# Kernel optimization log

Measured on AMD Instinct MI355X. Metric: run time of the kernel, lower is better.

The kernel has to match this reference:

```python
import jax, jax.numpy as jnp
import numpy as np
from jax import lax

B, L = 2, 2048          # batch, seq_len
V = 256                 # vocab
DM = 256                # d_model
DI = 512                # d_inner = 2*d_model (expand=2)
N = 16                  # d_state
R = 16                  # dt_rank = ceil(d_model/16)
K = 4                   # d_conv
NL = 4                  # n_layer
DO = 10                 # d_output
EPS = 1e-5


def setup_inputs() -> dict:
    key = jax.random.key(0)
    ks = jax.random.split(key, 12)
    f = lambda k, shp, s=0.02: (jax.random.normal(k, shp, jnp.float32) * s)
    A_init = jnp.log(jnp.tile(jnp.arange(1, N + 1, dtype=jnp.float32)[None, None, :], (NL, DI, 1)))
    return {
        "input_ids": jax.random.randint(ks[0], (B, L), 0, V, dtype=jnp.int32),
        "emb": f(ks[1], (V, DM)),
        "norm_w": jnp.ones((NL, DM), jnp.float32),
        "norm_b": jnp.zeros((NL, DM), jnp.float32),
        "in_proj_w": f(ks[2], (NL, 2 * DI, DM)),
        "conv_w": f(ks[3], (NL, DI, K), 0.1),
        "conv_b": jnp.zeros((NL, DI), jnp.float32),
        "x_proj_w": f(ks[4], (NL, R + 2 * N, DI)),
        "dt_proj_w": f(ks[5], (NL, DI, R), 0.1),
        "dt_proj_b": f(ks[6], (NL, DI), 0.1),
        "A_log": A_init,
        "Dp": jnp.ones((NL, DI), jnp.float32),
        "out_proj_w": f(ks[7], (NL, DM, DI)),
        "normf_w": jnp.ones((DM,), jnp.float32),
        "normf_b": jnp.zeros((DM,), jnp.float32),
        "dec_w": f(ks[8], (DO, DM)),
        "dec_b": jnp.zeros((DO,), jnp.float32),
    }


def _layer_norm(x, w, b):
    m = x.mean(-1, keepdims=True)
    v = jnp.mean((x - m) ** 2, axis=-1, keepdims=True)
    return (x - m) * lax.rsqrt(v + EPS) * w + b


def _causal_dwconv(x, w, b):
    # x: [B,L,DI], w: [DI,K] depthwise causal conv
    xt = x.transpose(0, 2, 1)  # [B,DI,L]
    out = lax.conv_general_dilated(xt, w[:, None, :], (1,), [(K - 1, 0)],
                                   feature_group_count=DI)
    return (out + b[None, :, None]).transpose(0, 2, 1)


def _selective_scan(deltaA, deltaBu, C):
    # deltaA, deltaBu: [B,L,DI,N]; C: [B,L,N]
    def step(h, inp):
        dA, dBu, c = inp
        h = dA * h + dBu                       # [B,DI,N]
        y = jnp.einsum('bdn,bn->bd', h, c)
        return h, y
    h0 = jnp.zeros(deltaA.shape[:1] + deltaA.shape[2:], deltaA.dtype)
    _, ys = lax.scan(step, h0, (deltaA.transpose(1, 0, 2, 3),
                                deltaBu.transpose(1, 0, 2, 3),
                                C.transpose(1, 0, 2)))
    return ys.transpose(1, 0, 2)  # [B,L,DI]


def _mixer(x, in_w, cw, cb, xp_w, dt_w, dt_b, A_log, Dp, out_w):
    xz = jnp.einsum('bld,ed->ble', x, in_w)        # [B,L,2*DI]
    xm, z = jnp.split(xz, 2, axis=-1)
    xc = jax.nn.silu(_causal_dwconv(xm, cw, cb))   # [B,L,DI]
    x_dbl = jnp.einsum('bld,ed->ble', xc, xp_w)    # [B,L,R+2N]
    dt, Bm, Cm = jnp.split(x_dbl, [R, R + N], axis=-1)
    delta = jax.nn.softplus(jnp.einsum('blr,dr->bld', dt, dt_w) + dt_b)  # [B,L,DI]
    A = -jnp.exp(A_log)                            # [DI,N]
    deltaA = jnp.exp(delta[..., None] * A)         # [B,L,DI,N]
    deltaBu = delta[..., None] * Bm[:, :, None, :] * xc[..., None]
    y = _selective_scan(deltaA, deltaBu, Cm)       # [B,L,DI]
    y = y + Dp * xc
    y = y * jax.nn.silu(z)
    return jnp.einsum('bld,ed->ble', y, out_w)     # [B,L,DM]


def reference(input_ids, emb, norm_w, norm_b, in_proj_w, conv_w, conv_b,
              x_proj_w, dt_proj_w, dt_proj_b, A_log, Dp, out_proj_w,
              normf_w, normf_b, dec_w, dec_b):
    hidden = emb[input_ids]                        # [B,L,DM]
    residual = None
    for i in range(NL):
        residual = hidden + residual if residual is not None else hidden
        h = _layer_norm(residual, norm_w[i], norm_b[i])
        hidden = _mixer(h, in_proj_w[i], conv_w[i], conv_b[i], x_proj_w[i],
                        dt_proj_w[i], dt_proj_b[i], A_log[i], Dp[i], out_proj_w[i])
    residual = hidden + residual
    hidden = _layer_norm(residual, normf_w, normf_b)
    pooled = hidden.mean(axis=1)                   # [B,DM]
    return pooled @ dec_w.T + dec_b                # [B,DO]
```

## Files before the change

kernel.cpp:

```cpp
#include <hip/hip_runtime.h>
#include <hip/hip_bf16.h>

#define BB 2
#define LL 2048
#define DM 256
#define DI 512
#define NST 16
#define RDT 16
#define KC 4
#define NLAY 4
#define DOUT 10
#define XDIM 48
#define TOK (BB*LL)
#define EPSF 1e-5f
#define CHUNK 16
#define NCH (LL/CHUNK)

typedef __bf16 bf16x8 __attribute__((ext_vector_type(8)));
typedef __bf16 bf16x4 __attribute__((ext_vector_type(4)));
typedef float  f32x4  __attribute__((ext_vector_type(4)));

__device__ __forceinline__ float sigmoid_f(float x) { return 1.0f / (1.0f + __expf(-x)); }

__global__ void cast_w_kernel(const float* __restrict__ a, const float* __restrict__ b,
                              const float* __restrict__ c,
                              __bf16* __restrict__ ab, __bf16* __restrict__ bb,
                              __bf16* __restrict__ cbf,
                              int na, int nb, int nc) {
  int stride = gridDim.x * 256;
  for (int i = blockIdx.x*256 + threadIdx.x; i < na; i += stride) ab[i] = (__bf16)a[i];
  for (int i = blockIdx.x*256 + threadIdx.x; i < nb; i += stride) bb[i] = (__bf16)b[i];
  for (int i = blockIdx.x*256 + threadIdx.x; i < nc; i += stride) cbf[i] = (__bf16)c[i];
}

__global__ void add_ln_kernel(float* __restrict__ residual, const float* __restrict__ hidden,
                              const int* __restrict__ ids, const float* __restrict__ emb,
                              const float* __restrict__ w, const float* __restrict__ bia,
                              float* __restrict__ out, __bf16* __restrict__ out_bf,
                              int first, int write32) {
  int t = blockIdx.x, d = threadIdx.x;
  __shared__ float ws8[8];
  float r;
  if (first) r = emb[ids[t]*DM + d];
  else       r = hidden[t*DM + d] + residual[t*DM + d];
  residual[t*DM + d] = r;
  float s = r;
  #pragma unroll
  for (int o = 32; o; o >>= 1) s += __shfl_down(s, o);
  if ((d & 63) == 0) ws8[d >> 6] = s;
  __syncthreads();
  float mean = (ws8[0] + ws8[1] + ws8[2] + ws8[3]) * (1.0f/DM);
  float diff = r - mean;
  float q = diff * diff;
  #pragma unroll
  for (int o = 32; o; o >>= 1) q += __shfl_down(q, o);
  if ((d & 63) == 0) ws8[4 + (d >> 6)] = q;
  __syncthreads();
  float var = (ws8[4] + ws8[5] + ws8[6] + ws8[7]) * (1.0f/DM);
  float v = diff * rsqrtf(var + EPSF) * w[d] + bia[d];
  if (write32) out[t*DM + d] = v;
  out_bf[t*DM + d] = (__bf16)v;
}

__global__ __launch_bounds__(256, 2) void gemm_in_bf16(const __bf16* __restrict__ A,
                                                       const __bf16* __restrict__ W,
                                                       __bf16* __restrict__ xm,
                                                       __bf16* __restrict__ zg) {
  __shared__ __bf16 As[4*64*8];
  __shared__ __bf16 Ws[8*64*8];
  const int K = DM;
  int tid = threadIdx.x;
  int lane = tid & 63, wv = tid >> 6;
  int bm = blockIdx.y * 64, be = blockIdx.x * 128;
  int ss = tid >> 6, sq = (tid >> 4) & 3, sm = tid & 15;
  f32x4 acc[8];
  #pragma unroll
  for (int et = 0; et < 8; ++et) acc[et] = (f32x4){0.f, 0.f, 0.f, 0.f};
  for (int k0 = 0; k0 < K; k0 += 32) {
    bf16x8 av = *(const bf16x8*)&A[(size_t)(bm + ss*16 + sm)*K + k0 + sq*8];
    bf16x8 w0 = *(const bf16x8*)&W[(size_t)(be + ss*16 + sm)*K + k0 + sq*8];
    bf16x8 w1 = *(const bf16x8*)&W[(size_t)(be + 64 + ss*16 + sm)*K + k0 + sq*8];
    __syncthreads();
    *(bf16x8*)&As[((ss*4 + sq)*16 + sm)*8] = av;
    *(bf16x8*)&Ws[((ss*4 + sq)*16 + sm)*8] = w0;
    *(bf16x8*)&Ws[(((4 + ss)*4 + sq)*16 + sm)*8] = w1;
    __syncthreads();
    bf16x8 af = *(const bf16x8*)&As[(wv*64 + lane)*8];
    #pragma unroll
    for (int et = 0; et < 8; ++et) {
      bf16x8 bfr = *(const bf16x8*)&Ws[(et*64 + lane)*8];
      acc[et] = __builtin_amdgcn_mfma_f32_16x16x32_bf16(af, bfr, acc[et], 0, 0, 0);
    }
  }
  int row0 = bm + wv*16 + (lane >> 4)*4;
  int colb = lane & 15;
  #pragma unroll
  for (int et = 0; et < 8; ++et) {
    int col = be + et*16 + colb;
    if (col < DI) {
      #pragma unroll
      for (int r = 0; r < 4; ++r)
        xm[(size_t)(row0 + r)*DI + col] = (__bf16)acc[et][r];
    } else {
      #pragma unroll
      for (int r = 0; r < 4; ++r) {
        float zv = acc[et][r];
        zg[(size_t)(row0 + r)*DI + col - DI] = (__bf16)(zv * sigmoid_f(zv));
      }
    }
  }
}

__global__ __launch_bounds__(256, 2) void gemm_out_bf16(const __bf16* __restrict__ A,
                                                        const __bf16* __restrict__ W,
                                                        float* __restrict__ C) {
  __shared__ __bf16 As[4*64*8];
  __shared__ __bf16 Ws[4*64*8];
  const int K = DI, E = DM;
  int tid = threadIdx.x;
  int lane = tid & 63, wv = tid >> 6;
  int bm = blockIdx.y * 64, be = blockIdx.x * 64;
  int ss = tid >> 6, sq = (tid >> 4) & 3, sm = tid & 15;
  f32x4 acc[4];
  #pragma unroll
  for (int et = 0; et < 4; ++et) acc[et] = (f32x4){0.f, 0.f, 0.f, 0.f};
  for (int k0 = 0; k0 < K; k0 += 32) {
    bf16x8 av = *(const bf16x8*)&A[(size_t)(bm + ss*16 + sm)*K + k0 + sq*8];
    bf16x8 wvv = *(const bf16x8*)&W[(size_t)(be + ss*16 + sm)*K + k0 + sq*8];
    __syncthreads();
    *(bf16x8*)&As[((ss*4 + sq)*16 + sm)*8] = av;
    *(bf16x8*)&Ws[((ss*4 + sq)*16 + sm)*8] = wvv;
    __syncthreads();
    bf16x8 af = *(const bf16x8*)&As[(wv*64 + lane)*8];
    #pragma unroll
    for (int et = 0; et < 4; ++et) {
      bf16x8 bfr = *(const bf16x8*)&Ws[(et*64 + lane)*8];
      acc[et] = __builtin_amdgcn_mfma_f32_16x16x32_bf16(af, bfr, acc[et], 0, 0, 0);
    }
  }
  int row0 = bm + wv*16 + (lane >> 4)*4;
  int col0 = be + (lane & 15);
  #pragma unroll
  for (int et = 0; et < 4; ++et)
    #pragma unroll
    for (int r = 0; r < 4; ++r)
      C[(size_t)(row0 + r)*E + col0 + et*16] = acc[et][r];
}

__global__ __launch_bounds__(512, 2) void xproj16(const __bf16* __restrict__ xm,
                                                  const float* __restrict__ cw,
                                                  const float* __restrict__ cb,
                                                  const __bf16* __restrict__ Wbf,
                                                  float* __restrict__ out,
                                                  __bf16* __restrict__ xc) {
  __shared__ float red[8][3][16][16];
  int tid = threadIdx.x;
  int lane = tid & 63, w = tid >> 6;
  int bm = blockIdx.x * 16;
  int row = bm + (lane & 15);
  int l = row & (LL - 1);
  int kg = (lane >> 4) * 8;
  f32x4 acc[3];
  #pragma unroll
  for (int e = 0; e < 3; ++e) acc[e] = (f32x4){0.f, 0.f, 0.f, 0.f};
  #pragma unroll
  for (int ks = 0; ks < 2; ++ks) {
    int ch = w*64 + ks*32 + kg;
    bf16x8 v0 = *(const bf16x8*)&xm[(size_t)row*DI + ch];
    bf16x8 v1 = (l >= 1) ? *(const bf16x8*)&xm[(size_t)(row-1)*DI + ch] : (bf16x8)(__bf16)0;
    bf16x8 v2 = (l >= 2) ? *(const bf16x8*)&xm[(size_t)(row-2)*DI + ch] : (bf16x8)(__bf16)0;
    bf16x8 v3 = (l >= 3) ? *(const bf16x8*)&xm[(size_t)(row-3)*DI + ch] : (bf16x8)(__bf16)0;
    bf16x8 a8;
    #pragma unroll
    for (int j = 0; j < 8; ++j) {
      float4 cwv = *(const float4*)&cw[(ch + j)*KC];
      float cv = cb[ch + j];
      cv = fmaf(cwv.x, (float)v3[j], cv);
      cv = fmaf(cwv.y, (float)v2[j], cv);
      cv = fmaf(cwv.z, (float)v1[j], cv);
      cv = fmaf(cwv.w, (float)v0[j], cv);
      a8[j] = (__bf16)(cv * sigmoid_f(cv));
    }
    *(bf16x8*)&xc[(size_t)row*DI + ch] = a8;
    #pragma unroll
    for (int e = 0; e < 3; ++e) {
      bf16x8 bv = *(const bf16x8*)&Wbf[(size_t)(e*16 + (lane & 15))*DI + ch];
      acc[e] = __builtin_amdgcn_mfma_f32_16x16x32_bf16(a8, bv, acc[e], 0, 0, 0);
    }
  }
  #pragma unroll
  for (int e = 0; e < 3; ++e)
    #pragma unroll
    for (int r = 0; r < 4; ++r)
      red[w][e][(lane >> 4)*4 + r][lane & 15] = acc[e][r];
  __syncthreads();
  for (int idx = tid; idx < 768; idx += 512) {
    int e = idx >> 8, rr = (idx >> 4) & 15, cc = idx & 15;
    float s = 0.f;
    #pragma unroll
    for (int w8 = 0; w8 < 8; ++w8) s += red[w8][e][rr][cc];
    out[(size_t)(bm + rr)*XDIM + e*16 + cc] = s;
  }
}

__global__ __launch_bounds__(256) void scan_pass1(
    const __bf16* __restrict__ xc, const float* __restrict__ xdbl,
    const float* __restrict__ dtw, const float* __restrict__ dtb,
    const float* __restrict__ A_log, const float* __restrict__ Dp,
    float* __restrict__ hloc, float* __restrict__ dsum,
    float* __restrict__ ylocal, float* __restrict__ csout) {
  __shared__ __align__(16) float DBC[CHUNK][48];
  int bc = blockIdx.x >> 1;
  int d  = ((blockIdx.x & 1) << 8) + threadIdx.x;
  int b = bc >> 7, c = bc & (NCH-1);
  int t0 = b*LL + c*CHUNK;
  int tid = threadIdx.x;
  if (tid < CHUNK*12) {
    int row = tid / 12, q = tid - row*12;
    *(float4*)&DBC[row][q*4] = *(const float4*)&xdbl[(size_t)(t0+row)*XDIM + q*4];
  }
  __syncthreads();
  float4 wq[4];
  #pragma unroll
  for (int i = 0; i < 4; ++i) wq[i] = *(const float4*)&dtw[(size_t)d*RDT + i*4];
  float dtbv = dtb[d];
  float Dpv = Dp[d];
  float A[NST];
  #pragma unroll
  for (int n = 0; n < NST; ++n) A[n] = -__expf(A_log[d*NST + n]);
  float A0 = A[0];
  bool geo = true;
  #pragma unroll
  for (int n = 1; n < NST; ++n) {
    float ideal = A0 * (float)(n+1);
    geo = geo && (fabsf(A[n] - ideal) <= 1e-5f * fabsf(ideal));
  }
  float h[NST];
  #pragma unroll
  for (int n = 0; n < NST; ++n) h[n] = 0.f;
  float ds = 0.f;
  for (int l = 0; l < CHUNK; ++l) {
    int t = t0 + l;
    float xcv = (float)xc[(size_t)t*DI + d];
    float acc = dtbv;
    #pragma unroll
    for (int i = 0; i < 4; ++i) {
      float4 a = *(const float4*)&DBC[l][i*4];
      acc = fmaf(a.x, wq[i].x, acc); acc = fmaf(a.y, wq[i].y, acc);
      acc = fmaf(a.z, wq[i].z, acc); acc = fmaf(a.w, wq[i].w, acc);
    }
    float del = fmaxf(acc, 0.f) + log1pf(__expf(-fabsf(acc)));
    ds += del;
    float dx = del * xcv;
    float yv = 0.f;
    if (geo) {
      float e = __expf(del * A0);
      float dA = e;
      h[0] = fmaf(dA, h[0], dx * DBC[l][16]);
      yv = fmaf(h[0], DBC[l][32], yv);
      #pragma unroll
      for (int n = 1; n < NST; ++n) {
        dA *= e;
        h[n] = fmaf(dA, h[n], dx * DBC[l][16 + n]);
        yv = fmaf(h[n], DBC[l][32 + n], yv);
      }
    } else {
      #pragma unroll
      for (int n = 0; n < NST; ++n) {
        h[n] = fmaf(__expf(del * A[n]), h[n], dx * DBC[l][16 + n]);
        yv = fmaf(h[n], DBC[l][32 + n], yv);
      }
    }
    yv = fmaf(Dpv, xcv, yv);
    ylocal[(size_t)t*DI + d] = yv;
    csout[(size_t)t*DI + d] = ds;
  }
  #pragma unroll
  for (int n = 0; n < NST; ++n)
    hloc[((size_t)(b*NST + n)*NCH + c)*DI + d] = h[n];
  dsum[(size_t)bc*DI + d] = ds;
}

__global__ __launch_bounds__(256) void scan_pass2(
    const float* __restrict__ hloc, const float* __restrict__ dsum,
    const float* __restrict__ A_log, float* __restrict__ hinit) {
  int g = blockIdx.x*256 + threadIdx.x;
  int d = g & (DI-1);
  int n = (g >> 9) & (NST-1);
  int b = g >> 13;
  float A = -__expf(A_log[d*NST + n]);
  float hc = 0.f;
  size_t base = (size_t)(b*NST + n)*NCH*DI + d;
  #pragma unroll 4
  for (int c = 0; c < NCH; ++c) {
    hinit[base + (size_t)c*DI] = hc;
    float P = __expf(A * dsum[(size_t)(b*NCH + c)*DI + d]);
    hc = fmaf(P, hc, hloc[base + (size_t)c*DI]);
  }
}

__global__ __launch_bounds__(256) void scan_pass3(
    const float* __restrict__ cs, const float* __restrict__ ylocal,
    const __bf16* __restrict__ zg, const float* __restrict__ xdbl,
    const float* __restrict__ A_log, const float* __restrict__ hinit,
    __bf16* __restrict__ y) {
  __shared__ __align__(16) float Cs[CHUNK][16];
  int bc = blockIdx.x >> 1;
  int d  = ((blockIdx.x & 1) << 8) + threadIdx.x;
  int b = bc >> 7, c = bc & (NCH-1);
  int t0 = b*LL + c*CHUNK;
  int tid = threadIdx.x;
  if (tid < CHUNK*4) {
    int row = tid >> 2, q = tid & 3;
    *(float4*)&Cs[row][q*4] = *(const float4*)&xdbl[(size_t)(t0+row)*XDIM + 32 + q*4];
  }
  __syncthreads();
  float A[NST];
  #pragma unroll
  for (int n = 0; n < NST; ++n) A[n] = -__expf(A_log[d*NST + n]);
  float A0 = A[0];
  bool geo = true;
  #pragma unroll
  for (int n = 1; n < NST; ++n) {
    float ideal = A0 * (float)(n+1);
    geo = geo && (fabsf(A[n] - ideal) <= 1e-5f * fabsf(ideal));
  }
  float hin[NST];
  #pragma unroll
  for (int n = 0; n < NST; ++n) hin[n] = hinit[((size_t)(b*NST + n)*NCH + c)*DI + d];
  for (int l = 0; l < CHUNK; ++l) {
    int t = t0 + l;
    float csv = cs[(size_t)t*DI + d];
    float ylv = ylocal[(size_t)t*DI + d];
    float zvg = (float)zg[(size_t)t*DI + d];
    float corr = 0.f;
    if (geo) {
      float g = __expf(csv * A0);
      float dA = g;
      corr = hin[0] * dA * Cs[l][0];
      #pragma unroll
      for (int n = 1; n < NST; ++n) {
        dA *= g;
        corr = fmaf(hin[n] * dA, Cs[l][n], corr);
      }
    } else {
      #pragma unroll
      for (int n = 0; n < NST; ++n)
        corr = fmaf(hin[n] * __expf(A[n] * csv), Cs[l][n], corr);
    }
    y[(size_t)t*DI + d] = (__bf16)((ylv + corr) * zvg);
  }
}

__global__ void pool1_kernel(const float* __restrict__ ln, float* __restrict__ part) {
  int blk = blockIdx.x;
  int b = blk >> 7, c = blk & 127;
  int d = threadIdx.x;
  const float* base = ln + (size_t)b*LL*DM + (size_t)c*16*DM + d;
  float s = 0.f;
  #pragma unroll
  for (int l = 0; l < 16; ++l) s += base[(size_t)l*DM];
  part[(size_t)blk*DM + d] = s;
}

__global__ void pool_decode_kernel(const float* __restrict__ part, const float* __restrict__ dw,
                                   const float* __restrict__ db, float* __restrict__ out) {
  int b = blockIdx.x, d = threadIdx.x;
  __shared__ float pooled[DM];
  float s = 0.f;
  for (int c = 0; c < 128; ++c) s += part[(size_t)(b*128 + c)*DM + d];
  pooled[d] = s * (1.0f/LL);
  __syncthreads();
  if (d < DOUT) {
    float acc = db[d];
    for (int m = 0; m < DM; ++m) acc = fmaf(pooled[m], dw[d*DM + m], acc);
    out[b*DOUT + d] = acc;
  }
}

extern "C" void kernel_launch(void* const* d_in, const int* in_sizes, int n_in,
                              void* d_out, int out_size, void* d_ws, size_t ws_size,
                              hipStream_t stream) {
  const int*   ids     = (const int*)d_in[0];
  const float* emb     = (const float*)d_in[1];
  const float* norm_w  = (const float*)d_in[2];
  const float* norm_b  = (const float*)d_in[3];
  const float* in_w    = (const float*)d_in[4];
  const float* conv_w  = (const float*)d_in[5];
  const float* conv_b  = (const float*)d_in[6];
  const float* xp_w    = (const float*)d_in[7];
  const float* dt_w    = (const float*)d_in[8];
  const float* dt_b    = (const float*)d_in[9];
  const float* A_log   = (const float*)d_in[10];
  const float* Dp      = (const float*)d_in[11];
  const float* out_w   = (const float*)d_in[12];
  const float* normf_w = (const float*)d_in[13];
  const float* normf_b = (const float*)d_in[14];
  const float* dec_w   = (const float*)d_in[15];
  const float* dec_b   = (const float*)d_in[16];
  float* out = (float*)d_out;

  float* ws = (float*)d_ws;
  float* hidden   = ws; ws += TOK*DM;
  float* residual = ws; ws += TOK*DM;
  float* hbuf     = ws; ws += TOK*DM;
  float* xdblbuf  = ws; ws += TOK*XDIM;
  float* hlocbuf  = ws; ws += (size_t)BB*NCH*NST*DI;
  float* hinitbuf = ws; ws += (size_t)BB*NCH*NST*DI;
  float* dsumbuf  = ws; ws += (size_t)BB*NCH*DI;
  float* partbuf  = ws; ws += (size_t)BB*128*DM;
  float* csbuf    = ws; ws += (size_t)TOK*DI;
  float* ylbuf    = ws; ws += (size_t)TOK*DI;
  __bf16* xmbuf   = (__bf16*)ws; ws += TOK*DI/2;
  __bf16* zgbuf   = (__bf16*)ws; ws += TOK*DI/2;
  __bf16* xcbuf   = (__bf16*)ws; ws += TOK*DI/2;
  __bf16* hbuf_bf = (__bf16*)ws; ws += TOK*DM/2;
  __bf16* ybuf_bf = (__bf16*)ws; ws += TOK*DI/2;
  __bf16* inw_bf  = (__bf16*)ws; ws += (size_t)NLAY*2*DI*DM/2;
  __bf16* outw_bf = (__bf16*)ws; ws += (size_t)NLAY*DM*DI/2;
  __bf16* xpw_bf  = (__bf16*)ws; ws += (size_t)NLAY*XDIM*DI/2 + 256;

  const int n_inw = NLAY*2*DI*DM, n_outw = NLAY*DM*DI, n_xpw = NLAY*XDIM*DI;
  cast_w_kernel<<<2048, 256, 0, stream>>>(in_w, out_w, xp_w, inw_bf, outw_bf, xpw_bf,
                                          n_inw, n_outw, n_xpw);

  for (int i = 0; i < NLAY; ++i) {
    add_ln_kernel<<<TOK, DM, 0, stream>>>(residual, hidden, ids, emb,
                                          norm_w + i*DM, norm_b + i*DM,
                                          hbuf, hbuf_bf, i == 0, 0);
    gemm_in_bf16<<<dim3((2*DI)/128, TOK/64), 256, 0, stream>>>(
        hbuf_bf, inw_bf + (size_t)i*2*DI*DM, xmbuf, zgbuf);
    xproj16<<<TOK/16, 512, 0, stream>>>(
        xmbuf, conv_w + i*DI*KC, conv_b + i*DI,
        xpw_bf + (size_t)i*XDIM*DI, xdblbuf, xcbuf);
    scan_pass1<<<BB*NCH*(DI/256), 256, 0, stream>>>(
        xcbuf, xdblbuf,
        dt_w + (size_t)i*DI*RDT, dt_b + i*DI, A_log + (size_t)i*DI*NST,
        Dp + i*DI, hlocbuf, dsumbuf, ylbuf, csbuf);
    scan_pass2<<<(BB*NST*DI)/256, 256, 0, stream>>>(
        hlocbuf, dsumbuf, A_log + (size_t)i*DI*NST, hinitbuf);
    scan_pass3<<<BB*NCH*(DI/256), 256, 0, stream>>>(
        csbuf, ylbuf, zgbuf, xdblbuf, A_log + (size_t)i*DI*NST,
        hinitbuf, ybuf_bf);
    gemm_out_bf16<<<dim3(DM/64, TOK/64), 256, 0, stream>>>(
        ybuf_bf, outw_bf + (size_t)i*DM*DI, hidden);
  }

  add_ln_kernel<<<TOK, DM, 0, stream>>>(residual, hidden, ids, emb,
                                        normf_w, normf_b, hbuf, hbuf_bf, 0, 1);
  pool1_kernel<<<BB*128, DM, 0, stream>>>(hbuf, partbuf);
  pool_decode_kernel<<<BB, DM, 0, stream>>>(partbuf, dec_w, dec_b, out);
}
```

Before: 432.5 us.

## Replace LDS-tiled GEMMs with direct-load MFMA kernels and shrink scan_pass2 blocks

The in-projection and out-projection GEMMs drop shared-memory staging and barriers. Each wave now loads its A and W fragments straight from global memory into MFMA operands, using 16-row tiles and more blocks. scan_pass2 uses 64-thread blocks so its 16384 threads spread over more CUs. The aim is to remove sync and LDS overhead and raise parallelism, at the cost of redundant global and L2 reads of the weight fragments across blocks.

```diff
diff --git a/kernel.cpp b/kernel.cpp
--- a/kernel.cpp
+++ b/kernel.cpp
@@ -62,89 +62,74 @@
   out_bf[t*DM + d] = (__bf16)v;
 }
 
-__global__ __launch_bounds__(256, 2) void gemm_in_bf16(const __bf16* __restrict__ A,
-                                                       const __bf16* __restrict__ W,
-                                                       __bf16* __restrict__ xm,
-                                                       __bf16* __restrict__ zg) {
-  __shared__ __bf16 As[4*64*8];
-  __shared__ __bf16 Ws[8*64*8];
-  const int K = DM;
+__global__ __launch_bounds__(512, 4) void gemm_in_d(const __bf16* __restrict__ A,
+                                                    const __bf16* __restrict__ W,
+                                                    __bf16* __restrict__ xm,
+                                                    __bf16* __restrict__ zg) {
   int tid = threadIdx.x;
   int lane = tid & 63, wv = tid >> 6;
-  int bm = blockIdx.y * 64, be = blockIdx.x * 128;
-  int ss = tid >> 6, sq = (tid >> 4) & 3, sm = tid & 15;
-  f32x4 acc[8];
-  #pragma unroll
-  for (int et = 0; et < 8; ++et) acc[et] = (f32x4){0.f, 0.f, 0.f, 0.f};
-  for (int k0 = 0; k0 < K; k0 += 32) {
-    bf16x8 av = *(const bf16x8*)&A[(size_t)(bm + ss*16 + sm)*K + k0 + sq*8];
-    bf16x8 w0 = *(const bf16x8*)&W[(size_t)(be + ss*16 + sm)*K + k0 + sq*8];
-    bf16x8 w1 = *(const bf16x8*)&W[(size_t)(be + 64 + ss*16 + sm)*K + k0 + sq*8];
-    __syncthreads();
-    *(bf16x8*)&As[((ss*4 + sq)*16 + sm)*8] = av;
-    *(bf16x8*)&Ws[((ss*4 + sq)*16 + sm)*8] = w0;
-    *(bf16x8*)&Ws[(((4 + ss)*4 + sq)*16 + sm)*8] = w1;
-    __syncthreads();
-    bf16x8 af = *(const bf16x8*)&As[(wv*64 + lane)*8];
-    #pragma unroll
-    for (int et = 0; et < 8; ++et) {
-      bf16x8 bfr = *(const bf16x8*)&Ws[(et*64 + lane)*8];
-      acc[et] = __builtin_amdgcn_mfma_f32_16x16x32_bf16(af, bfr, acc[et], 0, 0, 0);
-    }
-  }
-  int row0 = bm + wv*16 + (lane >> 4)*4;
-  int colb = lane & 15;
-  #pragma unroll
-  for (int et = 0; et < 8; ++et) {
-    int col = be + et*16 + colb;
-    if (col < DI) {
+  int bm = blockIdx.y * 16;
+  int row = bm + (lane & 15);
+  int kg = (lane >> 4) * 8;
+  int be = blockIdx.x * 512 + wv * 64;
+  f32x4 acc[4];
+  #pragma unroll
+  for (int e = 0; e < 4; ++e) acc[e] = (f32x4){0.f, 0.f, 0.f, 0.f};
+  for (int k0 = 0; k0 < DM; k0 += 32) {
+    bf16x8 av = *(const bf16x8*)&A[(size_t)row*DM + k0 + kg];
+    #pragma unroll
+    for (int e = 0; e < 4; ++e) {
+      bf16x8 bv = *(const bf16x8*)&W[(size_t)(be + e*16 + (lane & 15))*DM + k0 + kg];
+      acc[e] = __builtin_amdgcn_mfma_f32_16x16x32_bf16(av, bv, acc[e], 0, 0, 0);
+    }
+  }
+  int r0 = bm + (lane >> 4)*4;
+  int cb = lane & 15;
+  if (blockIdx.x == 0) {
+    #pragma unroll
+    for (int e = 0; e < 4; ++e)
       #pragma unroll
       for (int r = 0; r < 4; ++r)
-        xm[(size_t)(row0 + r)*DI + col] = (__bf16)acc[et][r];
-    } else {
+        xm[(size_t)(r0 + r)*DI + be + e*16 + cb] = (__bf16)acc[e][r];
+  } else {
+    int ze = be - DI;
+    #pragma unroll
+    for (int e = 0; e < 4; ++e)
       #pragma unroll
       for (int r = 0; r < 4; ++r) {
-        float zv = acc[et][r];
-        zg[(size_t)(row0 + r)*DI + col - DI] = (__bf16)(zv * sigmoid_f(zv));
+        float zv = acc[e][r];
+        zg[(size_t)(r0 + r)*DI + ze + e*16 + cb] = (__bf16)(zv * sigmoid_f(zv));
       }
-    }
-  }
-}
-
-__global__ __launch_bounds__(256, 2) void gemm_out_bf16(const __bf16* __restrict__ A,
-                                                        const __bf16* __restrict__ W,
-                                                        float* __restrict__ C) {
-  __shared__ __bf16 As[4*64*8];
-  __shared__ __bf16 Ws[4*64*8];
-  const int K = DI, E = DM;
+  }
+}
+
+__global__ __launch_bounds__(256, 4) void gemm_out_d(const __bf16* __restrict__ A,
+                                                     const __bf16* __restrict__ W,
+                                                     float* __restrict__ C) {
   int tid = threadIdx.x;
   int lane = tid & 63, wv = tid >> 6;
-  int bm = blockIdx.y * 64, be = blockIdx.x * 64;
-  int ss = tid >> 6, sq = (tid >> 4) & 3, sm = tid & 15;
-  f32x4 acc[4];
-  #pragma unroll
-  for (int et = 0; et < 4; ++et) acc[et] = (f32x4){0.f, 0.f, 0.f, 0.f};
-  for (int k0 = 0; k0 < K; k0 += 32) {
-    bf16x8 av = *(const bf16x8*)&A[(size_t)(bm + ss*16 + sm)*K + k0 + sq*8];
-    bf16x8 wvv = *(const bf16x8*)&W[(size_t)(be + ss*16 + sm)*K + k0 + sq*8];
-    __syncthreads();
-    *(bf16x8*)&As[((ss*4 + sq)*16 + sm)*8] = av;
-    *(bf16x8*)&Ws[((ss*4 + sq)*16 + sm)*8] = wvv;
-    __syncthreads();
-    bf16x8 af = *(const bf16x8*)&As[(wv*64 + lane)*8];
-    #pragma unroll
-    for (int et = 0; et < 4; ++et) {
-      bf16x8 bfr = *(const bf16x8*)&Ws[(et*64 + lane)*8];
-      acc[et] = __builtin_amdgcn_mfma_f32_16x16x32_bf16(af, bfr, acc[et], 0, 0, 0);
-    }
-  }
-  int row0 = bm + wv*16 + (lane >> 4)*4;
-  int col0 = be + (lane & 15);
-  #pragma unroll
-  for (int et = 0; et < 4; ++et)
+  int bm = blockIdx.y * 16;
+  int row = bm + (lane & 15);
+  int kg = (lane >> 4) * 8;
+  int be = blockIdx.x * 128 + wv * 32;
+  f32x4 acc[2];
+  #pragma unroll
+  for (int e = 0; e < 2; ++e) acc[e] = (f32x4){0.f, 0.f, 0.f, 0.f};
+  for (int k0 = 0; k0 < DI; k0 += 32) {
+    bf16x8 av = *(const bf16x8*)&A[(size_t)row*DI + k0 + kg];
+    #pragma unroll
+    for (int e = 0; e < 2; ++e) {
+      bf16x8 bv = *(const bf16x8*)&W[(size_t)(be + e*16 + (lane & 15))*DI + k0 + kg];
+      acc[e] = __builtin_amdgcn_mfma_f32_16x16x32_bf16(av, bv, acc[e], 0, 0, 0);
+    }
+  }
+  int r0 = bm + (lane >> 4)*4;
+  int cb = lane & 15;
+  #pragma unroll
+  for (int e = 0; e < 2; ++e)
     #pragma unroll
     for (int r = 0; r < 4; ++r)
-      C[(size_t)(row0 + r)*E + col0 + et*16] = acc[et][r];
+      C[(size_t)(r0 + r)*DM + be + e*16 + cb] = acc[e][r];
 }
 
 __global__ __launch_bounds__(512, 2) void xproj16(const __bf16* __restrict__ xm,
@@ -281,10 +266,10 @@
   dsum[(size_t)bc*DI + d] = ds;
 }
 
-__global__ __launch_bounds__(256) void scan_pass2(
+__global__ __launch_bounds__(64) void scan_pass2(
     const float* __restrict__ hloc, const float* __restrict__ dsum,
     const float* __restrict__ A_log, float* __restrict__ hinit) {
-  int g = blockIdx.x*256 + threadIdx.x;
+  int g = blockIdx.x*64 + threadIdx.x;
   int d = g & (DI-1);
   int n = (g >> 9) & (NST-1);
   int b = g >> 13;
@@ -428,7 +413,7 @@
     add_ln_kernel<<<TOK, DM, 0, stream>>>(residual, hidden, ids, emb,
                                           norm_w + i*DM, norm_b + i*DM,
                                           hbuf, hbuf_bf, i == 0, 0);
-    gemm_in_bf16<<<dim3((2*DI)/128, TOK/64), 256, 0, stream>>>(
+    gemm_in_d<<<dim3(2, TOK/16), 512, 0, stream>>>(
         hbuf_bf, inw_bf + (size_t)i*2*DI*DM, xmbuf, zgbuf);
     xproj16<<<TOK/16, 512, 0, stream>>>(
         xmbuf, conv_w + i*DI*KC, conv_b + i*DI,
@@ -437,12 +422,12 @@
         xcbuf, xdblbuf,
         dt_w + (size_t)i*DI*RDT, dt_b + i*DI, A_log + (size_t)i*DI*NST,
         Dp + i*DI, hlocbuf, dsumbuf, ylbuf, csbuf);
-    scan_pass2<<<(BB*NST*DI)/256, 256, 0, stream>>>(
+    scan_pass2<<<(BB*NST*DI)/64, 64, 0, stream>>>(
         hlocbuf, dsumbuf, A_log + (size_t)i*DI*NST, hinitbuf);
     scan_pass3<<<BB*NCH*(DI/256), 256, 0, stream>>>(
         csbuf, ylbuf, zgbuf, xdblbuf, A_log + (size_t)i*DI*NST,
         hinitbuf, ybuf_bf);
-    gemm_out_bf16<<<dim3(DM/64, TOK/64), 256, 0, stream>>>(
+    gemm_out_d<<<dim3(2, TOK/16), 256, 0, stream>>>(
         ybuf_bf, outw_bf + (size_t)i*DM*DI, hidden);
   }
 
```

Measured after the change: 482.0 us. 11.5% more time.

## Fuse conv/x-projection with first scan pass, keep xc in shared memory

Applied to the files above, without the earlier changes.

Merges the conv+SiLU+x_proj kernel with the chunk-local scan pass so each 512-thread block handles one 16-token chunk. The conv output xc stays in XOR-swizzled shared memory and the x_proj results go straight into the shared DBC tile, so xc no longer makes a round trip through global memory and one kernel launch per layer goes away. Separately, scan_pass2 now uses 64-thread blocks to spread its 16K threads over more workgroups. The cost is a fused kernel with more shared memory, no occupancy hint in its launch bounds, and 512 threads per block doing the sequential scan, which may lower occupancy.

```diff
diff --git a/kernel.cpp b/kernel.cpp
--- a/kernel.cpp
+++ b/kernel.cpp
@@ -147,19 +147,27 @@
       C[(size_t)(row0 + r)*E + col0 + et*16] = acc[et][r];
 }
 
-__global__ __launch_bounds__(512, 2) void xproj16(const __bf16* __restrict__ xm,
-                                                  const float* __restrict__ cw,
-                                                  const float* __restrict__ cb,
-                                                  const __bf16* __restrict__ Wbf,
-                                                  float* __restrict__ out,
-                                                  __bf16* __restrict__ xc) {
+__global__ __launch_bounds__(512) void xproj_scan1(
+    const __bf16* __restrict__ xm, const float* __restrict__ cw,
+    const float* __restrict__ cb, const __bf16* __restrict__ Wbf,
+    const float* __restrict__ dtw, const float* __restrict__ dtb,
+    const float* __restrict__ A_log, const float* __restrict__ Dp,
+    float* __restrict__ xdbl, float* __restrict__ hloc,
+    float* __restrict__ dsum, float* __restrict__ ylocal,
+    float* __restrict__ csout) {
   __shared__ float red[8][3][16][16];
+  __shared__ __bf16 xc_s[CHUNK][DI];
+  __shared__ __align__(16) float DBC[CHUNK][48];
   int tid = threadIdx.x;
   int lane = tid & 63, w = tid >> 6;
-  int bm = blockIdx.x * 16;
-  int row = bm + (lane & 15);
+  int bc = blockIdx.x;
+  int t0 = bc * CHUNK;
+  int b = bc >> 7, c = bc & (NCH - 1);
+  int r16 = lane & 15;
+  int row = t0 + r16;
   int l = row & (LL - 1);
   int kg = (lane >> 4) * 8;
+
   f32x4 acc[3];
   #pragma unroll
   for (int e = 0; e < 3; ++e) acc[e] = (f32x4){0.f, 0.f, 0.f, 0.f};
@@ -181,10 +189,10 @@
       cv = fmaf(cwv.w, (float)v0[j], cv);
       a8[j] = (__bf16)(cv * sigmoid_f(cv));
     }
-    *(bf16x8*)&xc[(size_t)row*DI + ch] = a8;
+    *(bf16x8*)&xc_s[r16][ch ^ ((r16 & 7) << 3)] = a8;
     #pragma unroll
     for (int e = 0; e < 3; ++e) {
-      bf16x8 bv = *(const bf16x8*)&Wbf[(size_t)(e*16 + (lane & 15))*DI + ch];
+      bf16x8 bv = *(const bf16x8*)&Wbf[(size_t)(e*16 + r16)*DI + ch];
       acc[e] = __builtin_amdgcn_mfma_f32_16x16x32_bf16(a8, bv, acc[e], 0, 0, 0);
     }
   }
@@ -192,34 +200,19 @@
   for (int e = 0; e < 3; ++e)
     #pragma unroll
     for (int r = 0; r < 4; ++r)
-      red[w][e][(lane >> 4)*4 + r][lane & 15] = acc[e][r];
+      red[w][e][(lane >> 4)*4 + r][r16] = acc[e][r];
   __syncthreads();
   for (int idx = tid; idx < 768; idx += 512) {
     int e = idx >> 8, rr = (idx >> 4) & 15, cc = idx & 15;
     float s = 0.f;
     #pragma unroll
     for (int w8 = 0; w8 < 8; ++w8) s += red[w8][e][rr][cc];
-    out[(size_t)(bm + rr)*XDIM + e*16 + cc] = s;
-  }
-}
-
-__global__ __launch_bounds__(256) void scan_pass1(
-    const __bf16* __restrict__ xc, const float* __restrict__ xdbl,
-    const float* __restrict__ dtw, const float* __restrict__ dtb,
-    const float* __restrict__ A_log, const float* __restrict__ Dp,
-    float* __restrict__ hloc, float* __restrict__ dsum,
-    float* __restrict__ ylocal, float* __restrict__ csout) {
-  __shared__ __align__(16) float DBC[CHUNK][48];
-  int bc = blockIdx.x >> 1;
-  int d  = ((blockIdx.x & 1) << 8) + threadIdx.x;
-  int b = bc >> 7, c = bc & (NCH-1);
-  int t0 = b*LL + c*CHUNK;
-  int tid = threadIdx.x;
-  if (tid < CHUNK*12) {
-    int row = tid / 12, q = tid - row*12;
-    *(float4*)&DBC[row][q*4] = *(const float4*)&xdbl[(size_t)(t0+row)*XDIM + q*4];
-  }
-  __syncthreads();
+    DBC[rr][e*16 + cc] = s;
+    xdbl[(size_t)(t0 + rr)*XDIM + e*16 + cc] = s;
+  }
+  __syncthreads();
+
+  int d = tid;
   float4 wq[4];
   #pragma unroll
   for (int i = 0; i < 4; ++i) wq[i] = *(const float4*)&dtw[(size_t)d*RDT + i*4];
@@ -239,36 +232,36 @@
   #pragma unroll
   for (int n = 0; n < NST; ++n) h[n] = 0.f;
   float ds = 0.f;
-  for (int l = 0; l < CHUNK; ++l) {
-    int t = t0 + l;
-    float xcv = (float)xc[(size_t)t*DI + d];
-    float acc = dtbv;
+  for (int lp = 0; lp < CHUNK; ++lp) {
+    int t = t0 + lp;
+    float xcv = (float)xc_s[lp][d ^ ((lp & 7) << 3)];
+    float acs = dtbv;
     #pragma unroll
     for (int i = 0; i < 4; ++i) {
-      float4 a = *(const float4*)&DBC[l][i*4];
-      acc = fmaf(a.x, wq[i].x, acc); acc = fmaf(a.y, wq[i].y, acc);
-      acc = fmaf(a.z, wq[i].z, acc); acc = fmaf(a.w, wq[i].w, acc);
-    }
-    float del = fmaxf(acc, 0.f) + log1pf(__expf(-fabsf(acc)));
+      float4 a = *(const float4*)&DBC[lp][i*4];
+      acs = fmaf(a.x, wq[i].x, acs); acs = fmaf(a.y, wq[i].y, acs);
+      acs = fmaf(a.z, wq[i].z, acs); acs = fmaf(a.w, wq[i].w, acs);
+    }
+    float del = fmaxf(acs, 0.f) + log1pf(__expf(-fabsf(acs)));
     ds += del;
     float dx = del * xcv;
     float yv = 0.f;
     if (geo) {
       float e = __expf(del * A0);
       float dA = e;
-      h[0] = fmaf(dA, h[0], dx * DBC[l][16]);
-      yv = fmaf(h[0], DBC[l][32], yv);
+      h[0] = fmaf(dA, h[0], dx * DBC[lp][16]);
+      yv = fmaf(h[0], DBC[lp][32], yv);
       #pragma unroll
       for (int n = 1; n < NST; ++n) {
         dA *= e;
-        h[n] = fmaf(dA, h[n], dx * DBC[l][16 + n]);
-        yv = fmaf(h[n], DBC[l][32 + n], yv);
+        h[n] = fmaf(dA, h[n], dx * DBC[lp][16 + n]);
+        yv = fmaf(h[n], DBC[lp][32 + n], yv);
       }
     } else {
       #pragma unroll
       for (int n = 0; n < NST; ++n) {
-        h[n] = fmaf(__expf(del * A[n]), h[n], dx * DBC[l][16 + n]);
-        yv = fmaf(h[n], DBC[l][32 + n], yv);
+        h[n] = fmaf(__expf(del * A[n]), h[n], dx * DBC[lp][16 + n]);
+        yv = fmaf(h[n], DBC[lp][32 + n], yv);
       }
     }
     yv = fmaf(Dpv, xcv, yv);
@@ -281,10 +274,10 @@
   dsum[(size_t)bc*DI + d] = ds;
 }
 
-__global__ __launch_bounds__(256) void scan_pass2(
+__global__ __launch_bounds__(64) void scan_pass2(
     const float* __restrict__ hloc, const float* __restrict__ dsum,
     const float* __restrict__ A_log, float* __restrict__ hinit) {
-  int g = blockIdx.x*256 + threadIdx.x;
+  int g = blockIdx.x*64 + threadIdx.x;
   int d = g & (DI-1);
   int n = (g >> 9) & (NST-1);
   int b = g >> 13;
@@ -413,7 +406,6 @@
   float* ylbuf    = ws; ws += (size_t)TOK*DI;
   __bf16* xmbuf   = (__bf16*)ws; ws += TOK*DI/2;
   __bf16* zgbuf   = (__bf16*)ws; ws += TOK*DI/2;
-  __bf16* xcbuf   = (__bf16*)ws; ws += TOK*DI/2;
   __bf16* hbuf_bf = (__bf16*)ws; ws += TOK*DM/2;
   __bf16* ybuf_bf = (__bf16*)ws; ws += TOK*DI/2;
   __bf16* inw_bf  = (__bf16*)ws; ws += (size_t)NLAY*2*DI*DM/2;
@@ -430,14 +422,12 @@
                                           hbuf, hbuf_bf, i == 0, 0);
     gemm_in_bf16<<<dim3((2*DI)/128, TOK/64), 256, 0, stream>>>(
         hbuf_bf, inw_bf + (size_t)i*2*DI*DM, xmbuf, zgbuf);
-    xproj16<<<TOK/16, 512, 0, stream>>>(
+    xproj_scan1<<<TOK/CHUNK, 512, 0, stream>>>(
         xmbuf, conv_w + i*DI*KC, conv_b + i*DI,
-        xpw_bf + (size_t)i*XDIM*DI, xdblbuf, xcbuf);
-    scan_pass1<<<BB*NCH*(DI/256), 256, 0, stream>>>(
-        xcbuf, xdblbuf,
+        xpw_bf + (size_t)i*XDIM*DI,
         dt_w + (size_t)i*DI*RDT, dt_b + i*DI, A_log + (size_t)i*DI*NST,
-        Dp + i*DI, hlocbuf, dsumbuf, ylbuf, csbuf);
-    scan_pass2<<<(BB*NST*DI)/256, 256, 0, stream>>>(
+        Dp + i*DI, xdblbuf, hlocbuf, dsumbuf, ylbuf, csbuf);
+    scan_pass2<<<(BB*NST*DI)/64, 64, 0, stream>>>(
         hlocbuf, dsumbuf, A_log + (size_t)i*DI*NST, hinitbuf);
     scan_pass3<<<BB*NCH*(DI/256), 256, 0, stream>>>(
         csbuf, ylbuf, zgbuf, xdblbuf, A_log + (size_t)i*DI*NST,
```

Measured after the change: 417.4 us. -3.5%, faster.
